# Kernel tuning notes

Hardware: AMD Instinct MI355X
Metric: run time of the kernel (lower is better)

## Reference

```python
import jax, jax.numpy as jnp
import numpy as np

EPS = 1e-8


def _layer_norm(x, w, b):
    mu = jnp.mean(x, axis=-1, keepdims=True)
    var = jnp.mean((x - mu) ** 2, axis=-1, keepdims=True)
    return (x - mu) * jax.lax.rsqrt(var + EPS) * w + b


def setup_inputs() -> dict:
    key = jax.random.key(0)
    k1, k2, k3 = jax.random.split(key, 3)
    B, S, D = 8, 2048, 1024
    return {
        "x_real": jax.random.normal(k1, (B, S, D), dtype=jnp.float32),
        "x_imag": jax.random.normal(k2, (B, S, D), dtype=jnp.float32),
        "phase_matrix": jax.random.normal(k3, (D, D), dtype=jnp.float32) * 0.02,
        "coherence_factor": jnp.ones((1,), dtype=jnp.float32) * 0.1,
        "ln_weight": jnp.ones((D,), dtype=jnp.float32),
        "ln_bias": jnp.zeros((D,), dtype=jnp.float32),
    }


def reference(x_real, x_imag, phase_matrix, coherence_factor, ln_weight, ln_bias):
    D = x_real.shape[-1]
    # coherence = mean_{i,j} cos(phi_i - phi_j) over the last dim pairwise;
    # exact trig identity: sum_{i,j} cos(phi_i-phi_j) = (sum cos)^2 + (sum sin)^2
    phases = jnp.arctan2(x_imag + EPS, x_real + EPS)          # [B,S,D]
    sc = jnp.sum(jnp.cos(phases), axis=-1, keepdims=True)      # [B,S,1]
    ss = jnp.sum(jnp.sin(phases), axis=-1, keepdims=True)      # [B,S,1]
    coherence = (sc * sc + ss * ss) / (D * D)                  # [B,S,1]

    # phase rotation driven by GEMM
    phase_adjustment = jnp.einsum('bsd,de->bse', x_real, phase_matrix)
    phase_adjustment = phase_adjustment * coherence_factor * (1.0 - coherence)
    c, s = jnp.cos(phase_adjustment), jnp.sin(phase_adjustment)
    new_real = x_real * c - x_imag * s
    new_imag = x_real * s + x_imag * c

    # unit-modulus normalization
    norm = jnp.sqrt(new_real ** 2 + new_imag ** 2 + EPS)
    new_real = new_real / norm
    new_imag = new_imag / norm

    return (_layer_norm(new_real, ln_weight, ln_bias),
            _layer_norm(new_imag, ln_weight, ln_bias))
```

## Files before the change

kernel.cpp:

```cpp
#include <hip/hip_runtime.h>
#include <hip/hip_fp16.h>

#define DEV __device__ __forceinline__

typedef __bf16 bf16x8 __attribute__((ext_vector_type(8)));
typedef float f32x4 __attribute__((ext_vector_type(4)));
typedef short s16x8 __attribute__((ext_vector_type(8)));
typedef unsigned short u16;

static constexpr int D = 1024;
static constexpr int M = 16384;
static constexpr int R = 16;
static constexpr float EPS = 1e-8f;

static constexpr int B_OFF = 32768;
static constexpr int RED_OFF = 65536;
static constexpr int STATS_OFF = 67584;
static constexpr int SCALE_OFF = 67840;
static constexpr int SMEM_BYTES = 67904;

DEV u16 f2bf(float f) {
  union { float f; unsigned u; } v; v.f = f;
  unsigned u = v.u;
  return (u16)((u + 0x7FFFu + ((u >> 16) & 1u)) >> 16);
}

DEV void async_copy16(const void* g, void* l) {
  __builtin_amdgcn_global_load_lds(
      (const __attribute__((address_space(1))) void*)g,
      (__attribute__((address_space(3))) void*)l, 16, 0, 0);
}

union H2x4 { s16x8 v; __half2 h[4]; };

__global__ __launch_bounds__(256) void k_prep(const float* __restrict__ pm,
                                              u16* __restrict__ bt) {
  __shared__ float t[32][33];
  int bx = blockIdx.x * 32, by = blockIdx.y * 32;
  int tx = threadIdx.x, ty = threadIdx.y;
#pragma unroll
  for (int j = 0; j < 32; j += 8)
    t[ty + j][tx] = pm[(size_t)(by + ty + j) * D + bx + tx];
  __syncthreads();
#pragma unroll
  for (int j = 0; j < 32; j += 8) {
    int col = bx + ty + j, k = by + tx;
    int kk = k >> 5, nh = col >> 9, cb = (col >> 4) & 31, c15 = col & 15;
    int kg = (k >> 3) & 3, je = k & 7;
    bt[(size_t)(kk * 2 + nh) * 16384 + (size_t)((cb * 64 + kg * 16 + c15) * 8 + je)] =
        f2bf(t[tx][ty + j]);
  }
}

__global__ __launch_bounds__(512, 4) void k_fused(
    const float* __restrict__ xr, const float* __restrict__ xi,
    const u16* __restrict__ bt, const float* __restrict__ cfp,
    const float* __restrict__ lw, const float* __restrict__ lb,
    float* __restrict__ outR, float* __restrict__ outI) {
  __shared__ __align__(16) unsigned char smem[SMEM_BYTES];
  u16* A_lds = (u16*)smem;
  u16* B_u16 = (u16*)(smem + B_OFF);
  __half2* stash = (__half2*)smem;
  float* red = (float*)(smem + RED_OFF);
  float* stats = (float*)(smem + STATS_OFF);
  float* scale_s = (float*)(smem + SCALE_OFF);

  const int tid = threadIdx.x;
  const int lane = tid & 63;
  const int l15 = lane & 15, l4 = lane >> 4;
  const int wv = tid >> 6;
  const size_t row0 = (size_t)blockIdx.x * R;
  const float cfv = cfp[0];

  {
    int row = tid >> 5;
    int s32 = tid & 31;
    const float* xrp = xr + (row0 + row) * D;
    const float* xip = xi + (row0 + row) * D;
    float sc = 0.f, ss = 0.f;
#pragma unroll
    for (int it = 0; it < 4; ++it) {
      int kgl = it * 32 + s32;
      f32x4 a0 = *(const f32x4*)(xrp + kgl * 8);
      f32x4 a1 = *(const f32x4*)(xrp + kgl * 8 + 4);
      f32x4 b0 = *(const f32x4*)(xip + kgl * 8);
      f32x4 b1 = *(const f32x4*)(xip + kgl * 8 + 4);
      float fx[8] = {a0.x, a0.y, a0.z, a0.w, a1.x, a1.y, a1.z, a1.w};
      float fy[8] = {b0.x, b0.y, b0.z, b0.w, b1.x, b1.y, b1.z, b1.w};
      s16x8 v;
#pragma unroll
      for (int j = 0; j < 8; ++j) {
        float x = fx[j] + EPS, y = fy[j] + EPS;
        float inv = rsqrtf(x * x + y * y);
        sc += x * inv;
        ss += y * inv;
        v[j] = (short)f2bf(fx[j]);
      }
      int kk = kgl >> 2, kg = kgl & 3;
      int u = kk * 64 + kg * 16 + (row ^ (kk & 15));
      *(s16x8*)&A_lds[u * 8] = v;
    }
    sc += __shfl_xor(sc, 1, 64); sc += __shfl_xor(sc, 2, 64);
    sc += __shfl_xor(sc, 4, 64); sc += __shfl_xor(sc, 8, 64);
    sc += __shfl_xor(sc, 16, 64);
    ss += __shfl_xor(ss, 1, 64); ss += __shfl_xor(ss, 2, 64);
    ss += __shfl_xor(ss, 4, 64); ss += __shfl_xor(ss, 8, 64);
    ss += __shfl_xor(ss, 16, 64);
    if (s32 == 0) {
      float coh = (sc * sc + ss * ss) * (1.0f / (1024.0f * 1024.0f));
      scale_s[row] = cfv * (1.0f - coh);
    }
  }
  __syncthreads();

  f32x4 acc[8] = {};

  for (int kk = 0; kk < 32; ++kk) {
    int ua = kk * 64 + l4 * 16 + (l15 ^ (kk & 15));
    bf16x8 af = __builtin_bit_cast(bf16x8, *(const s16x8*)&A_lds[ua * 8]);
#pragma unroll
    for (int nh = 0; nh < 2; ++nh) {
      const u16* src = bt + (size_t)(kk * 2 + nh) * 16384;
#pragma unroll
      for (int r = 0; r < 4; ++r) {
        int off = (r * 8 + wv) * 512 + lane * 8;
        async_copy16(src + off, B_u16 + off);
      }
      __syncthreads();
      __builtin_amdgcn_s_setprio(1);
#pragma unroll
      for (int nf = 0; nf < 4; ++nf) {
        int ub = (wv * 4 + nf) * 64 + l4 * 16 + l15;
        bf16x8 bf = __builtin_bit_cast(bf16x8, *(const s16x8*)&B_u16[ub * 8]);
        acc[nh * 4 + nf] =
            __builtin_amdgcn_mfma_f32_16x16x32_bf16(af, bf, acc[nh * 4 + nf], 0, 0, 0);
      }
      __builtin_amdgcn_s_setprio(0);
      __syncthreads();
    }
  }

  float srow4[4];
#pragma unroll
  for (int i = 0; i < 4; ++i) srow4[i] = scale_s[l4 * 4 + i];

  float s_r[4], q_r[4], s_i[4], q_i[4];
#pragma unroll
  for (int i = 0; i < 4; ++i) { s_r[i] = 0.f; q_r[i] = 0.f; s_i[i] = 0.f; q_i[i] = 0.f; }
#pragma unroll
  for (int i = 0; i < 4; ++i) {
    const int row_l = l4 * 4 + i;
    const float scl = srow4[i];
    const float* ar = xr + (row0 + row_l) * D;
    const float* ai = xi + (row0 + row_l) * D;
#pragma unroll
    for (int q = 0; q < 8; ++q) {
      int col = (q >> 2) * 512 + wv * 64 + (q & 3) * 16 + l15;
      float a = ar[col], b = ai[col];
      float t = acc[q][i] * scl;
      float t2 = t * t;
      float sn = t * (1.f + t2 * (-1.f / 6.f + t2 * (1.f / 120.f - t2 * (1.f / 5040.f))));
      float cs = 1.f + t2 * (-0.5f + t2 * (1.f / 24.f - t2 * (1.f / 720.f)));
      float nr = a * cs - b * sn;
      float ni = a * sn + b * cs;
      float inv = rsqrtf(nr * nr + ni * ni + EPS);
      nr *= inv; ni *= inv;
      int colx = col ^ ((row_l & 3) << 4);
      stash[row_l * 1024 + colx] = __floats2half2_rn(nr, ni);
      s_r[i] += nr; q_r[i] += nr * nr;
      s_i[i] += ni; q_i[i] += ni * ni;
    }
  }
#pragma unroll
  for (int i = 0; i < 4; ++i)
#pragma unroll
    for (int d = 1; d < 16; d <<= 1) {
      s_r[i] += __shfl_xor(s_r[i], d, 64);
      q_r[i] += __shfl_xor(q_r[i], d, 64);
      s_i[i] += __shfl_xor(s_i[i], d, 64);
      q_i[i] += __shfl_xor(q_i[i], d, 64);
    }
  if (l15 == 0) {
#pragma unroll
    for (int i = 0; i < 4; ++i) {
      int row_l = l4 * 4 + i;
      red[(row_l * 8 + wv) * 4 + 0] = s_r[i];
      red[(row_l * 8 + wv) * 4 + 1] = q_r[i];
      red[(row_l * 8 + wv) * 4 + 2] = s_i[i];
      red[(row_l * 8 + wv) * 4 + 3] = q_i[i];
    }
  }
  __syncthreads();
  if (wv == 0 && l15 == 0) {
#pragma unroll
    for (int i = 0; i < 4; ++i) {
      int row_l = l4 * 4 + i;
      float s0 = 0.f, s1 = 0.f, s2 = 0.f, s3 = 0.f;
#pragma unroll
      for (int w8 = 0; w8 < 8; ++w8) {
        s0 += red[(row_l * 8 + w8) * 4 + 0];
        s1 += red[(row_l * 8 + w8) * 4 + 1];
        s2 += red[(row_l * 8 + w8) * 4 + 2];
        s3 += red[(row_l * 8 + w8) * 4 + 3];
      }
      float mu_r = s0 * (1.f / 1024.f);
      float mu_i = s2 * (1.f / 1024.f);
      stats[row_l * 4 + 0] = mu_r;
      stats[row_l * 4 + 1] = rsqrtf(s1 * (1.f / 1024.f) - mu_r * mu_r + EPS);
      stats[row_l * 4 + 2] = mu_i;
      stats[row_l * 4 + 3] = rsqrtf(s3 * (1.f / 1024.f) - mu_i * mu_i + EPS);
    }
  }
  __syncthreads();

  {
    int row = tid >> 5, cg = tid & 31;
    float mu_r = stats[row * 4 + 0], rd_r = stats[row * 4 + 1];
    float mu_i = stats[row * 4 + 2], rd_i = stats[row * 4 + 3];
    float* orp = outR + (row0 + row) * D;
    float* oip = outI + (row0 + row) * D;
#pragma unroll
    for (int v = 0; v < 8; ++v) {
      int col = v * 128 + cg * 4;
      int colx = col ^ ((row & 3) << 4);
      H2x4 hv;
      hv.v = *(const s16x8*)&stash[row * 1024 + colx];
      f32x4 w4 = *(const f32x4*)(lw + col);
      f32x4 b4 = *(const f32x4*)(lb + col);
      f32x4 o_r, o_i;
#pragma unroll
      for (int j = 0; j < 4; ++j) {
        float nr = __low2float(hv.h[j]), ni = __high2float(hv.h[j]);
        o_r[j] = (nr - mu_r) * rd_r * w4[j] + b4[j];
        o_i[j] = (ni - mu_i) * rd_i * w4[j] + b4[j];
      }
      *(f32x4*)(orp + col) = o_r;
      *(f32x4*)(oip + col) = o_i;
    }
  }
}

extern "C" void kernel_launch(void* const* d_in, const int* in_sizes, int n_in,
                              void* d_out, int out_size, void* d_ws, size_t ws_size,
                              hipStream_t stream) {
  const float* xr = (const float*)d_in[0];
  const float* xi = (const float*)d_in[1];
  const float* pm = (const float*)d_in[2];
  const float* cf = (const float*)d_in[3];
  const float* lw = (const float*)d_in[4];
  const float* lb = (const float*)d_in[5];
  float* outR = (float*)d_out;
  float* outI = outR + (size_t)M * D;
  u16* bt = (u16*)d_ws;

  k_prep<<<dim3(32, 32), dim3(32, 8), 0, stream>>>(pm, bt);
  k_fused<<<M / R, 512, 0, stream>>>(xr, xi, bt, cf, lw, lb, outR, outI);
}
```

Measured before the change: 150.3 us.

## Double rows per block to reuse each B tile across two MFMA row blocks

Each block now processes 32 rows instead of 16, so every B tile streamed into LDS feeds two MFMA row groups. This halves B traffic from global memory and the count of barriers per row. The A tile only fits half of K in LDS, so the second half is reloaded from global and converted at kk==16 behind an extra barrier. The epilogue runs twice, once per 16-row half, reusing the stash. The cost is more accumulator registers, half as many blocks, and a mid-loop stall.

```diff
diff --git a/kernel.cpp b/kernel.cpp
--- a/kernel.cpp
+++ b/kernel.cpp
@@ -10,14 +10,14 @@
 
 static constexpr int D = 1024;
 static constexpr int M = 16384;
-static constexpr int R = 16;
+static constexpr int R = 32;
 static constexpr float EPS = 1e-8f;
 
 static constexpr int B_OFF = 32768;
 static constexpr int RED_OFF = 65536;
 static constexpr int STATS_OFF = 67584;
 static constexpr int SCALE_OFF = 67840;
-static constexpr int SMEM_BYTES = 67904;
+static constexpr int SMEM_BYTES = 67968;
 
 DEV u16 f2bf(float f) {
   union { float f; unsigned u; } v; v.f = f;
@@ -72,15 +72,16 @@
   const size_t row0 = (size_t)blockIdx.x * R;
   const float cfv = cfp[0];
 
+  const int prow = tid >> 4;
+  const int s16 = tid & 15;
+  const float* xrp = xr + (row0 + prow) * D;
+  const float* xip = xi + (row0 + prow) * D;
+
   {
-    int row = tid >> 5;
-    int s32 = tid & 31;
-    const float* xrp = xr + (row0 + row) * D;
-    const float* xip = xi + (row0 + row) * D;
     float sc = 0.f, ss = 0.f;
 #pragma unroll
-    for (int it = 0; it < 4; ++it) {
-      int kgl = it * 32 + s32;
+    for (int it = 0; it < 8; ++it) {
+      int kgl = it * 16 + s16;
       f32x4 a0 = *(const f32x4*)(xrp + kgl * 8);
       f32x4 a1 = *(const f32x4*)(xrp + kgl * 8 + 4);
       f32x4 b0 = *(const f32x4*)(xip + kgl * 8);
@@ -96,34 +97,54 @@
         ss += y * inv;
         v[j] = (short)f2bf(fx[j]);
       }
-      int kk = kgl >> 2, kg = kgl & 3;
-      int u = kk * 64 + kg * 16 + (row ^ (kk & 15));
-      *(s16x8*)&A_lds[u * 8] = v;
+      if (kgl < 64) {
+        int kq = kgl >> 2, kg = kgl & 3;
+        int u = kq * 128 + (prow >> 4) * 64 + kg * 16 + ((prow & 15) ^ kq);
+        *(s16x8*)&A_lds[u * 8] = v;
+      }
     }
     sc += __shfl_xor(sc, 1, 64); sc += __shfl_xor(sc, 2, 64);
     sc += __shfl_xor(sc, 4, 64); sc += __shfl_xor(sc, 8, 64);
-    sc += __shfl_xor(sc, 16, 64);
     ss += __shfl_xor(ss, 1, 64); ss += __shfl_xor(ss, 2, 64);
     ss += __shfl_xor(ss, 4, 64); ss += __shfl_xor(ss, 8, 64);
-    ss += __shfl_xor(ss, 16, 64);
-    if (s32 == 0) {
+    if (s16 == 0) {
       float coh = (sc * sc + ss * ss) * (1.0f / (1024.0f * 1024.0f));
-      scale_s[row] = cfv * (1.0f - coh);
+      scale_s[prow] = cfv * (1.0f - coh);
     }
   }
   __syncthreads();
 
-  f32x4 acc[8] = {};
+  f32x4 acc[2][8] = {};
 
   for (int kk = 0; kk < 32; ++kk) {
-    int ua = kk * 64 + l4 * 16 + (l15 ^ (kk & 15));
-    bf16x8 af = __builtin_bit_cast(bf16x8, *(const s16x8*)&A_lds[ua * 8]);
+    if (kk == 16) {
+#pragma unroll
+      for (int it = 0; it < 4; ++it) {
+        int kgl = 64 + it * 16 + s16;
+        f32x4 a0 = *(const f32x4*)(xrp + kgl * 8);
+        f32x4 a1 = *(const f32x4*)(xrp + kgl * 8 + 4);
+        float fx[8] = {a0.x, a0.y, a0.z, a0.w, a1.x, a1.y, a1.z, a1.w};
+        s16x8 v;
+#pragma unroll
+        for (int j = 0; j < 8; ++j) v[j] = (short)f2bf(fx[j]);
+        int kq = (kgl >> 2) & 15, kg = kgl & 3;
+        int u = kq * 128 + (prow >> 4) * 64 + kg * 16 + ((prow & 15) ^ kq);
+        *(s16x8*)&A_lds[u * 8] = v;
+      }
+      __syncthreads();
+    }
+    bf16x8 af[2];
+#pragma unroll
+    for (int rb = 0; rb < 2; ++rb) {
+      int u = (kk & 15) * 128 + rb * 64 + l4 * 16 + (l15 ^ (kk & 15));
+      af[rb] = __builtin_bit_cast(bf16x8, *(const s16x8*)&A_lds[u * 8]);
+    }
 #pragma unroll
     for (int nh = 0; nh < 2; ++nh) {
       const u16* src = bt + (size_t)(kk * 2 + nh) * 16384;
 #pragma unroll
       for (int r = 0; r < 4; ++r) {
-        int off = (r * 8 + wv) * 512 + lane * 8;
+        int off = ((r * 8 + wv) * 64 + lane) * 8;
         async_copy16(src + off, B_u16 + off);
       }
       __syncthreads();
@@ -132,111 +153,114 @@
       for (int nf = 0; nf < 4; ++nf) {
         int ub = (wv * 4 + nf) * 64 + l4 * 16 + l15;
         bf16x8 bf = __builtin_bit_cast(bf16x8, *(const s16x8*)&B_u16[ub * 8]);
-        acc[nh * 4 + nf] =
-            __builtin_amdgcn_mfma_f32_16x16x32_bf16(af, bf, acc[nh * 4 + nf], 0, 0, 0);
+        acc[0][nh * 4 + nf] =
+            __builtin_amdgcn_mfma_f32_16x16x32_bf16(af[0], bf, acc[0][nh * 4 + nf], 0, 0, 0);
+        acc[1][nh * 4 + nf] =
+            __builtin_amdgcn_mfma_f32_16x16x32_bf16(af[1], bf, acc[1][nh * 4 + nf], 0, 0, 0);
       }
       __builtin_amdgcn_s_setprio(0);
       __syncthreads();
     }
   }
 
-  float srow4[4];
-#pragma unroll
-  for (int i = 0; i < 4; ++i) srow4[i] = scale_s[l4 * 4 + i];
-
-  float s_r[4], q_r[4], s_i[4], q_i[4];
-#pragma unroll
-  for (int i = 0; i < 4; ++i) { s_r[i] = 0.f; q_r[i] = 0.f; s_i[i] = 0.f; q_i[i] = 0.f; }
-#pragma unroll
-  for (int i = 0; i < 4; ++i) {
-    const int row_l = l4 * 4 + i;
-    const float scl = srow4[i];
-    const float* ar = xr + (row0 + row_l) * D;
-    const float* ai = xi + (row0 + row_l) * D;
-#pragma unroll
-    for (int q = 0; q < 8; ++q) {
-      int col = (q >> 2) * 512 + wv * 64 + (q & 3) * 16 + l15;
-      float a = ar[col], b = ai[col];
-      float t = acc[q][i] * scl;
-      float t2 = t * t;
-      float sn = t * (1.f + t2 * (-1.f / 6.f + t2 * (1.f / 120.f - t2 * (1.f / 5040.f))));
-      float cs = 1.f + t2 * (-0.5f + t2 * (1.f / 24.f - t2 * (1.f / 720.f)));
-      float nr = a * cs - b * sn;
-      float ni = a * sn + b * cs;
-      float inv = rsqrtf(nr * nr + ni * ni + EPS);
-      nr *= inv; ni *= inv;
-      int colx = col ^ ((row_l & 3) << 4);
-      stash[row_l * 1024 + colx] = __floats2half2_rn(nr, ni);
-      s_r[i] += nr; q_r[i] += nr * nr;
-      s_i[i] += ni; q_i[i] += ni * ni;
-    }
-  }
-#pragma unroll
-  for (int i = 0; i < 4; ++i)
-#pragma unroll
-    for (int d = 1; d < 16; d <<= 1) {
-      s_r[i] += __shfl_xor(s_r[i], d, 64);
-      q_r[i] += __shfl_xor(q_r[i], d, 64);
-      s_i[i] += __shfl_xor(s_i[i], d, 64);
-      q_i[i] += __shfl_xor(q_i[i], d, 64);
-    }
-  if (l15 == 0) {
+#pragma unroll
+  for (int h = 0; h < 2; ++h) {
+    float s_r[4], q_r[4], s_i[4], q_i[4];
+#pragma unroll
+    for (int i = 0; i < 4; ++i) { s_r[i] = 0.f; q_r[i] = 0.f; s_i[i] = 0.f; q_i[i] = 0.f; }
 #pragma unroll
     for (int i = 0; i < 4; ++i) {
-      int row_l = l4 * 4 + i;
-      red[(row_l * 8 + wv) * 4 + 0] = s_r[i];
-      red[(row_l * 8 + wv) * 4 + 1] = q_r[i];
-      red[(row_l * 8 + wv) * 4 + 2] = s_i[i];
-      red[(row_l * 8 + wv) * 4 + 3] = q_i[i];
-    }
-  }
-  __syncthreads();
-  if (wv == 0 && l15 == 0) {
-#pragma unroll
-    for (int i = 0; i < 4; ++i) {
-      int row_l = l4 * 4 + i;
-      float s0 = 0.f, s1 = 0.f, s2 = 0.f, s3 = 0.f;
-#pragma unroll
-      for (int w8 = 0; w8 < 8; ++w8) {
-        s0 += red[(row_l * 8 + w8) * 4 + 0];
-        s1 += red[(row_l * 8 + w8) * 4 + 1];
-        s2 += red[(row_l * 8 + w8) * 4 + 2];
-        s3 += red[(row_l * 8 + w8) * 4 + 3];
-      }
-      float mu_r = s0 * (1.f / 1024.f);
-      float mu_i = s2 * (1.f / 1024.f);
-      stats[row_l * 4 + 0] = mu_r;
-      stats[row_l * 4 + 1] = rsqrtf(s1 * (1.f / 1024.f) - mu_r * mu_r + EPS);
-      stats[row_l * 4 + 2] = mu_i;
-      stats[row_l * 4 + 3] = rsqrtf(s3 * (1.f / 1024.f) - mu_i * mu_i + EPS);
-    }
-  }
-  __syncthreads();
-
-  {
-    int row = tid >> 5, cg = tid & 31;
-    float mu_r = stats[row * 4 + 0], rd_r = stats[row * 4 + 1];
-    float mu_i = stats[row * 4 + 2], rd_i = stats[row * 4 + 3];
-    float* orp = outR + (row0 + row) * D;
-    float* oip = outI + (row0 + row) * D;
-#pragma unroll
-    for (int v = 0; v < 8; ++v) {
-      int col = v * 128 + cg * 4;
-      int colx = col ^ ((row & 3) << 4);
-      H2x4 hv;
-      hv.v = *(const s16x8*)&stash[row * 1024 + colx];
-      f32x4 w4 = *(const f32x4*)(lw + col);
-      f32x4 b4 = *(const f32x4*)(lb + col);
-      f32x4 o_r, o_i;
-#pragma unroll
-      for (int j = 0; j < 4; ++j) {
-        float nr = __low2float(hv.h[j]), ni = __high2float(hv.h[j]);
-        o_r[j] = (nr - mu_r) * rd_r * w4[j] + b4[j];
-        o_i[j] = (ni - mu_i) * rd_i * w4[j] + b4[j];
-      }
-      *(f32x4*)(orp + col) = o_r;
-      *(f32x4*)(oip + col) = o_i;
-    }
+      const int row_l = l4 * 4 + i;
+      const int grow_l = h * 16 + row_l;
+      const float scl = scale_s[grow_l];
+      const float* ar = xr + (row0 + grow_l) * D;
+      const float* ai = xi + (row0 + grow_l) * D;
+      const int xm = ((row_l & 3) << 4) | (row_l & 12);
+#pragma unroll
+      for (int q = 0; q < 8; ++q) {
+        int col = (q >> 2) * 512 + wv * 64 + (q & 3) * 16 + l15;
+        float a = ar[col], b = ai[col];
+        float t = acc[h][q][i] * scl;
+        float t2 = t * t;
+        float sn = t * (1.f + t2 * (-1.f / 6.f + t2 * (1.f / 120.f - t2 * (1.f / 5040.f))));
+        float cs = 1.f + t2 * (-0.5f + t2 * (1.f / 24.f - t2 * (1.f / 720.f)));
+        float nr = a * cs - b * sn;
+        float ni = a * sn + b * cs;
+        float inv = rsqrtf(nr * nr + ni * ni + EPS);
+        nr *= inv; ni *= inv;
+        stash[row_l * 1024 + (col ^ xm)] = __floats2half2_rn(nr, ni);
+        s_r[i] += nr; q_r[i] += nr * nr;
+        s_i[i] += ni; q_i[i] += ni * ni;
+      }
+    }
+#pragma unroll
+    for (int i = 0; i < 4; ++i)
+#pragma unroll
+      for (int d = 1; d < 16; d <<= 1) {
+        s_r[i] += __shfl_xor(s_r[i], d, 64);
+        q_r[i] += __shfl_xor(q_r[i], d, 64);
+        s_i[i] += __shfl_xor(s_i[i], d, 64);
+        q_i[i] += __shfl_xor(q_i[i], d, 64);
+      }
+    if (l15 == 0) {
+#pragma unroll
+      for (int i = 0; i < 4; ++i) {
+        int row_l = l4 * 4 + i;
+        red[(row_l * 8 + wv) * 4 + 0] = s_r[i];
+        red[(row_l * 8 + wv) * 4 + 1] = q_r[i];
+        red[(row_l * 8 + wv) * 4 + 2] = s_i[i];
+        red[(row_l * 8 + wv) * 4 + 3] = q_i[i];
+      }
+    }
+    __syncthreads();
+    if (wv == 0 && l15 == 0) {
+#pragma unroll
+      for (int i = 0; i < 4; ++i) {
+        int row_l = l4 * 4 + i;
+        float s0 = 0.f, s1 = 0.f, s2 = 0.f, s3 = 0.f;
+#pragma unroll
+        for (int w8 = 0; w8 < 8; ++w8) {
+          s0 += red[(row_l * 8 + w8) * 4 + 0];
+          s1 += red[(row_l * 8 + w8) * 4 + 1];
+          s2 += red[(row_l * 8 + w8) * 4 + 2];
+          s3 += red[(row_l * 8 + w8) * 4 + 3];
+        }
+        float mu_r = s0 * (1.f / 1024.f);
+        float mu_i = s2 * (1.f / 1024.f);
+        stats[row_l * 4 + 0] = mu_r;
+        stats[row_l * 4 + 1] = rsqrtf(s1 * (1.f / 1024.f) - mu_r * mu_r + EPS);
+        stats[row_l * 4 + 2] = mu_i;
+        stats[row_l * 4 + 3] = rsqrtf(s3 * (1.f / 1024.f) - mu_i * mu_i + EPS);
+      }
+    }
+    __syncthreads();
+
+    {
+      int row = tid >> 5, cg = tid & 31;
+      int xm = ((row & 3) << 4) | (row & 12);
+      float mu_r = stats[row * 4 + 0], rd_r = stats[row * 4 + 1];
+      float mu_i = stats[row * 4 + 2], rd_i = stats[row * 4 + 3];
+      float* orp = outR + (row0 + h * 16 + row) * D;
+      float* oip = outI + (row0 + h * 16 + row) * D;
+#pragma unroll
+      for (int v = 0; v < 8; ++v) {
+        int col = v * 128 + cg * 4;
+        H2x4 hv;
+        hv.v = *(const s16x8*)&stash[row * 1024 + (col ^ xm)];
+        f32x4 w4 = *(const f32x4*)(lw + col);
+        f32x4 b4 = *(const f32x4*)(lb + col);
+        f32x4 o_r, o_i;
+#pragma unroll
+        for (int j = 0; j < 4; ++j) {
+          float nr = __low2float(hv.h[j]), ni = __high2float(hv.h[j]);
+          o_r[j] = (nr - mu_r) * rd_r * w4[j] + b4[j];
+          o_i[j] = (ni - mu_i) * rd_i * w4[j] + b4[j];
+        }
+        *(f32x4*)(orp + col) = o_r;
+        *(f32x4*)(oip + col) = o_i;
+      }
+    }
+    __syncthreads();
   }
 }
 
```

Result: slower. 169.3 us (+12.6%).
